# Performance work log

Measured on AMD Instinct MI355X. Metric: run time of the kernel, lower is better.

## Reference

```python
import jax, jax.numpy as jnp
import numpy as np


def setup_inputs() -> dict:
    key = jax.random.key(0)
    ks = jax.random.split(key, 5)
    B, S, D = 2, 2048, 1024
    std = 0.02
    return {
        "x": jax.random.normal(ks[0], (B, S, D), dtype=jnp.float32),
        "Wq": jax.random.normal(ks[1], (D, D), dtype=jnp.float32) * std,
        "Wk": jax.random.normal(ks[2], (D, D), dtype=jnp.float32) * std,
        "Wv": jax.random.normal(ks[3], (D, D), dtype=jnp.float32) * std,
        "Wo": jax.random.normal(ks[4], (D, D), dtype=jnp.float32) * std,
        "num_heads": 16,
        "window_size": 512,
    }


def reference(x, Wq, Wk, Wv, Wo, num_heads, window_size):
    B, S, D = x.shape
    H = num_heads
    d = D // H
    scale = d ** (-0.5)

    # QKV projections (torch Linear: y = x @ W.T), split heads -> b h s d
    def proj(W):
        return (x @ W.T).reshape(B, S, H, d).transpose(0, 2, 1, 3)

    q, k, v = proj(Wq), proj(Wk), proj(Wv)

    # [B, H, S, S] scores (faithful to the dense SDPA fallback)
    scores = jnp.einsum("bhsd,bhtd->bhst", q, k) * scale

    # sliding-window causal mask: col <= row and row - col < window_size
    pos = jnp.arange(S)
    row, col = pos[:, None], pos[None, :]
    mask = (col <= row) & (row - col < window_size)  # [S, S]
    scores = jnp.where(mask[None, None], scores, -jnp.inf)

    attn = jax.nn.softmax(scores, axis=-1)
    out = jnp.einsum("bhst,bhtd->bhsd", attn, v)  # b h s d
    out = out.transpose(0, 2, 1, 3).reshape(B, S, D)  # merge heads
    return out @ Wo.T
```

## Files before the change

### kernel.cpp

```cpp
#include <hip/hip_runtime.h>
#include <cstdint>

typedef uint16_t u16;
typedef __attribute__((ext_vector_type(8))) short short8;
typedef __attribute__((ext_vector_type(4))) float f32x4;

__device__ __forceinline__ u16 f2bf(float f) {
  uint32_t u = __float_as_uint(f);
  u += 0x7fff + ((u >> 16) & 1);
  return (u16)(u >> 16);
}
__device__ __forceinline__ uint32_t pk2bf(float a, float b) {
  uint32_t ua = __float_as_uint(a) + 0x8000u;
  uint32_t ub = __float_as_uint(b) + 0x8000u;
  return (ua >> 16) | (ub & 0xFFFF0000u);
}

#define GLL16(gp, lp) __builtin_amdgcn_global_load_lds( \
    (__attribute__((address_space(1))) void*)(gp), \
    (__attribute__((address_space(3))) void*)(lp), 16, 0, 0)

#define SBAR()       __builtin_amdgcn_s_barrier()
#define WAIT_LGKM0() asm volatile("s_waitcnt lgkmcnt(0)" ::: "memory")
#define WAIT_VM(N)   asm volatile("s_waitcnt vmcnt(" #N ")" ::: "memory")
#define MEMBAR()     asm volatile("" ::: "memory")

__global__ void cvt_all(const float* __restrict__ x,  const float* __restrict__ wq,
                        const float* __restrict__ wk, const float* __restrict__ wv,
                        const float* __restrict__ wo,
                        u16* __restrict__ xb, u16* __restrict__ wcat, u16* __restrict__ wob) {
  int i = blockIdx.x * 256 + threadIdx.x;
  const float4* src; ushort4* dst; int off; float sc = 1.0f;
  if (i < 1048576)      { src = (const float4*)x;  dst = (ushort4*)xb;              off = i; }
  else if (i < 1310720) { src = (const float4*)wq; dst = (ushort4*)wcat;            off = i - 1048576;
                          sc = 0.18033688011112042f; }
  else if (i < 1572864) { src = (const float4*)wk; dst = (ushort4*)wcat + 262144;   off = i - 1310720; }
  else if (i < 1835008) { src = (const float4*)wv; dst = (ushort4*)wcat + 524288;   off = i - 1572864; }
  else                  { src = (const float4*)wo; dst = (ushort4*)wob;             off = i - 1835008; }
  float4 v = src[off];
  ushort4 o;
  o.x = f2bf(v.x * sc); o.y = f2bf(v.y * sc); o.z = f2bf(v.z * sc); o.w = f2bf(v.w * sc);
  dst[off] = o;
}

template<int OUT_BF16>
__global__ __launch_bounds__(256, 2) void gemm128(const u16* __restrict__ A,
                                                  const u16* __restrict__ B,
                                                  void* __restrict__ Cout,
                                                  int N, int K, int ntN) {
  __shared__ u16 sm[2][2][128 * 64];
  const int tid  = threadIdx.x;
  const int lane = tid & 63, w = tid >> 6;
  const int wr = w >> 1, wc = w & 1;
  const int g = lane >> 4, lr = lane & 15;

  const int cpx = gridDim.x >> 3;
  const int id  = blockIdx.x;
  const int sw  = (id & 7) * cpx + (id >> 3);
  const int row0 = (sw / ntN) * 128, col0 = (sw % ntN) * 128;
  const int T = K >> 6;

  f32x4 acc[4][4];
  #pragma unroll
  for (int i = 0; i < 4; ++i)
    #pragma unroll
    for (int j = 0; j < 4; ++j) acc[i][j] = (f32x4){0.f, 0.f, 0.f, 0.f};

  auto STAGE = [&](int kt, int bufi) {
    #pragma unroll
    for (int ab = 0; ab < 2; ++ab) {
      const u16* __restrict__ src = ab ? B : A;
      const int rb = ab ? col0 : row0;
      #pragma unroll
      for (int j = 0; j < 4; ++j) {
        int r  = j * 32 + w * 8 + (lane >> 3);
        int sb = ((lane & 7) << 4) ^ ((r & 7) << 4);
        const u16* gp = src + (size_t)(rb + r) * K + kt * 64 + (sb >> 1);
        GLL16(gp, &sm[bufi][ab][(size_t)(j * 32 + w * 8) * 64]);
      }
    }
  };

  STAGE(0, 0); STAGE(1, 1);
  WAIT_VM(8); SBAR(); MEMBAR();

  for (int t = 0; t < T; ++t) {
    const int cur = t & 1;
    short8 a[4][2], b[4][2];
    #pragma unroll
    for (int mm = 0; mm < 4; ++mm)
      #pragma unroll
      for (int kh = 0; kh < 2; ++kh) {
        int row = wr * 64 + mm * 16 + lr;
        int col = (kh * 64 + g * 16) ^ ((row & 7) << 4);
        a[mm][kh] = *(const short8*)((const char*)&sm[cur][0][0] + row * 128 + col);
      }
    #pragma unroll
    for (int nn = 0; nn < 4; ++nn)
      #pragma unroll
      for (int kh = 0; kh < 2; ++kh) {
        int row = wc * 64 + nn * 16 + lr;
        int col = (kh * 64 + g * 16) ^ ((row & 7) << 4);
        b[nn][kh] = *(const short8*)((const char*)&sm[cur][1][0] + row * 128 + col);
      }
    WAIT_LGKM0(); MEMBAR(); SBAR(); MEMBAR();

    if (t + 2 < T) STAGE(t + 2, cur);

    __builtin_amdgcn_s_setprio(1);
    #pragma unroll
    for (int kh = 0; kh < 2; ++kh)
      #pragma unroll
      for (int mm = 0; mm < 4; ++mm)
        #pragma unroll
        for (int nn = 0; nn < 4; ++nn)
          acc[mm][nn] = __builtin_amdgcn_mfma_f32_16x16x32_bf16(
              a[mm][kh], b[nn][kh], acc[mm][nn], 0, 0, 0);
    __builtin_amdgcn_s_setprio(0);

    if (t + 1 < T) {
      if (t + 2 < T) { WAIT_VM(8); } else { WAIT_VM(0); }
      SBAR(); MEMBAR();
    }
  }

  #pragma unroll
  for (int i = 0; i < 4; ++i)
    #pragma unroll
    for (int j = 0; j < 4; ++j)
      #pragma unroll
      for (int ri = 0; ri < 4; ++ri) {
        int rr = row0 + wr * 64 + i * 16 + g * 4 + ri;
        int cc = col0 + wc * 64 + j * 16 + lr;
        if (OUT_BF16) ((u16*)Cout)[(size_t)rr * N + cc] = f2bf(acc[i][j][ri]);
        else          ((float*)Cout)[(size_t)rr * N + cc] = acc[i][j][ri];
      }
}

__global__ __launch_bounds__(256) void attn_swa(const u16* __restrict__ QKV, u16* __restrict__ O) {
  const int S = 2048;
  const int qb = blockIdx.x * 128;
  const int b = blockIdx.y >> 4, h = blockIdx.y & 15;
  const int tid = threadIdx.x;
  const int lane = tid & 63, w = tid >> 6;
  const int g = lane >> 4, lr = lane & 15;

  __shared__ u16 Klds[2][64 * 64];
  __shared__ u16 Vt[64][72];
  __shared__ u16 Plds[4][32][72];

  const u16* Qb = QKV + (size_t)b * S * 3072 + h * 64;
  const u16* Kb = QKV + (size_t)b * S * 3072 + 1024 + h * 64;
  const u16* Vb = QKV + (size_t)b * S * 3072 + 2048 + h * 64;

  const int qw = qb + w * 32;
  short8 qf[2][2];
  #pragma unroll
  for (int qg = 0; qg < 2; ++qg)
    #pragma unroll
    for (int kh = 0; kh < 2; ++kh)
      qf[qg][kh] = *(const short8*)(Qb + (size_t)(qw + qg * 16 + lr) * 3072 + kh * 32 + g * 8);

  float ls[2] = {0.f, 0.f};
  f32x4 accO[2][4];
  #pragma unroll
  for (int qg = 0; qg < 2; ++qg)
    #pragma unroll
    for (int i = 0; i < 4; ++i) accO[qg][i] = (f32x4){0.f, 0.f, 0.f, 0.f};

  int ks = qb - 511; if (ks < 0) ks = 0; ks &= ~63;
  const int ke = qb + 127;
  const int nt = ((ke - ks) >> 6) + 1;

  short8 vreg0, vreg1;

  auto STAGE_K = [&](int kb, int buf) {
    #pragma unroll
    for (int c = 0; c < 2; ++c) {
      int r  = c * 32 + w * 8 + (lane >> 3);
      int sb = ((lane & 7) << 4) ^ ((r & 7) << 4);
      const u16* gp = Kb + (size_t)(kb + r) * 3072 + (sb >> 1);
      u16* lp = Klds[buf] + c * 2048 + w * 512;
      GLL16(gp, lp);
    }
  };
  auto LOAD_V = [&](int kb) {
    vreg0 = *(const short8*)(Vb + (size_t)(kb + lane) * 3072 + w * 8);
    vreg1 = *(const short8*)(Vb + (size_t)(kb + lane) * 3072 + w * 8 + 32);
  };
  auto WRITE_V = [&]() {
    #pragma unroll
    for (int j = 0; j < 8; ++j) Vt[w * 8 + j][lane]      = (u16)vreg0[j];
    #pragma unroll
    for (int j = 0; j < 8; ++j) Vt[w * 8 + 32 + j][lane] = (u16)vreg1[j];
  };

  STAGE_K(ks, 0);
  LOAD_V(ks);
  __syncthreads();
  WRITE_V();
  __syncthreads();

  int cur = 0, kb = ks;
  for (int t = 0; t < nt; ++t, kb += 64) {
    const int nxt = cur ^ 1;
    const bool more = (t + 1 < nt);
    if (more) { STAGE_K(kb + 64, nxt); LOAD_V(kb + 64); }

    float p[2][4][4];
    #pragma unroll
    for (int st = 0; st < 4; ++st) {
      f32x4 c4[2];
      c4[0] = (f32x4){0.f, 0.f, 0.f, 0.f};
      c4[1] = (f32x4){0.f, 0.f, 0.f, 0.f};
      int r = st * 16 + lr;
      int swz = (r & 7) << 4;
      const char* krow = (const char*)(Klds[cur]) + r * 128;
      short8 kf0 = *(const short8*)(krow + ((g * 16) ^ swz));
      short8 kf1 = *(const short8*)(krow + ((64 + g * 16) ^ swz));
      __builtin_amdgcn_s_setprio(1);
      c4[0] = __builtin_amdgcn_mfma_f32_16x16x32_bf16(kf0, qf[0][0], c4[0], 0, 0, 0);
      c4[1] = __builtin_amdgcn_mfma_f32_16x16x32_bf16(kf0, qf[1][0], c4[1], 0, 0, 0);
      c4[0] = __builtin_amdgcn_mfma_f32_16x16x32_bf16(kf1, qf[0][1], c4[0], 0, 0, 0);
      c4[1] = __builtin_amdgcn_mfma_f32_16x16x32_bf16(kf1, qf[1][1], c4[1], 0, 0, 0);
      __builtin_amdgcn_s_setprio(0);
      #pragma unroll
      for (int ri = 0; ri < 4; ++ri) { p[0][st][ri] = c4[0][ri]; p[1][st][ri] = c4[1][ri]; }
    }

    #pragma unroll
    for (int qg = 0; qg < 2; ++qg) {
      const int q0 = qw + qg * 16;
      const bool clean = (kb + 63 <= q0) && (q0 + 15 - kb < 512);
      if (clean) {
        #pragma unroll
        for (int st = 0; st < 4; ++st)
          #pragma unroll
          for (int ri = 0; ri < 4; ++ri)
            p[qg][st][ri] = __builtin_amdgcn_exp2f(p[qg][st][ri]);
      } else {
        const int base = q0 + lr - kb;
        #pragma unroll
        for (int st = 0; st < 4; ++st)
          #pragma unroll
          for (int ri = 0; ri < 4; ++ri) {
            float e = __builtin_amdgcn_exp2f(p[qg][st][ri]);
            p[qg][st][ri] = ((uint32_t)(base - (st * 16 + g * 4 + ri)) < 512u) ? e : 0.f;
          }
      }
      float s = 0.f;
      #pragma unroll
      for (int st = 0; st < 4; ++st)
        #pragma unroll
        for (int ri = 0; ri < 4; ++ri) s += p[qg][st][ri];
      s += __shfl_xor(s, 16);
      s += __shfl_xor(s, 32);
      ls[qg] += s;

      #pragma unroll
      for (int st = 0; st < 4; ++st) {
        uint2 u2;
        u2.x = pk2bf(p[qg][st][0], p[qg][st][1]);
        u2.y = pk2bf(p[qg][st][2], p[qg][st][3]);
        *(uint2*)(&Plds[w][qg * 16 + lr][st * 16 + g * 4]) = u2;
      }
    }

    short8 pf[2][2];
    #pragma unroll
    for (int qg = 0; qg < 2; ++qg) {
      pf[qg][0] = *(const short8*)(&Plds[w][qg * 16 + lr][g * 8]);
      pf[qg][1] = *(const short8*)(&Plds[w][qg * 16 + lr][32 + g * 8]);
    }
    __builtin_amdgcn_s_setprio(1);
    #pragma unroll
    for (int dt = 0; dt < 4; ++dt) {
      short8 vf0 = *(const short8*)(&Vt[dt * 16 + lr][g * 8]);
      short8 vf1 = *(const short8*)(&Vt[dt * 16 + lr][32 + g * 8]);
      accO[0][dt] = __builtin_amdgcn_mfma_f32_16x16x32_bf16(pf[0][0], vf0, accO[0][dt], 0, 0, 0);
      accO[1][dt] = __builtin_amdgcn_mfma_f32_16x16x32_bf16(pf[1][0], vf0, accO[1][dt], 0, 0, 0);
      accO[0][dt] = __builtin_amdgcn_mfma_f32_16x16x32_bf16(pf[0][1], vf1, accO[0][dt], 0, 0, 0);
      accO[1][dt] = __builtin_amdgcn_mfma_f32_16x16x32_bf16(pf[1][1], vf1, accO[1][dt], 0, 0, 0);
    }
    __builtin_amdgcn_s_setprio(0);

    __syncthreads();
    if (more) WRITE_V();
    __syncthreads();
    cur = nxt;
  }

  #pragma unroll
  for (int qg = 0; qg < 2; ++qg) {
    float lsq[4];
    #pragma unroll
    for (int ri = 0; ri < 4; ++ri) lsq[ri] = __shfl(ls[qg], g * 4 + ri);
    #pragma unroll
    for (int dt = 0; dt < 4; ++dt)
      #pragma unroll
      for (int ri = 0; ri < 4; ++ri) {
        int qi = qw + qg * 16 + g * 4 + ri;
        O[(size_t)(b * S + qi) * 1024 + h * 64 + dt * 16 + lr] = f2bf(accO[qg][dt][ri] / lsq[ri]);
      }
  }
}

extern "C" void kernel_launch(void* const* d_in, const int* in_sizes, int n_in,
                              void* d_out, int out_size, void* d_ws, size_t ws_size,
                              hipStream_t stream) {
  const float* x  = (const float*)d_in[0];
  const float* Wq = (const float*)d_in[1];
  const float* Wk = (const float*)d_in[2];
  const float* Wv = (const float*)d_in[3];
  const float* Wo = (const float*)d_in[4];

  char* ws = (char*)d_ws;
  u16* xb   = (u16*)(ws);
  u16* Wcat = (u16*)(ws + (8  << 20));
  u16* Wob  = (u16*)(ws + (14 << 20));
  u16* QKV  = (u16*)(ws + (16 << 20));
  u16* Oatt = (u16*)(ws + (40 << 20));

  cvt_all<<<8192, 256, 0, stream>>>(x, Wq, Wk, Wv, Wo, xb, Wcat, Wob);
  gemm128<1><<<768, 256, 0, stream>>>(xb, Wcat, QKV, 3072, 1024, 24);
  attn_swa<<<dim3(16, 32), 256, 0, stream>>>(QKV, Oatt);
  gemm128<0><<<256, 256, 0, stream>>>(Oatt, Wob, d_out, 1024, 1024, 8);
}
```

Measured before the change: 91.01 us.

## Double-buffer V tile in LDS and drop one barrier per attention iteration

The transposed V tile in LDS is now double-buffered, so the next tile can be written while the current one is still being read. This removes the barrier that guarded the write-after-read and leaves a single barrier per iteration. The V global loads are reordered ahead of the K async LDS copies so that explicit vmcnt waits can target the V data alone. An occupancy hint of 3 blocks per CU is added to launch bounds. The extra LDS for the second V buffer and the register cap from the hint could limit occupancy or cause spills.

```diff
diff --git a/kernel.cpp b/kernel.cpp
--- a/kernel.cpp
+++ b/kernel.cpp
@@ -137,7 +137,7 @@
       }
 }
 
-__global__ __launch_bounds__(256) void attn_swa(const u16* __restrict__ QKV, u16* __restrict__ O) {
+__global__ __launch_bounds__(256, 3) void attn_swa(const u16* __restrict__ QKV, u16* __restrict__ O) {
   const int S = 2048;
   const int qb = blockIdx.x * 128;
   const int b = blockIdx.y >> 4, h = blockIdx.y & 15;
@@ -146,7 +146,7 @@
   const int g = lane >> 4, lr = lane & 15;
 
   __shared__ u16 Klds[2][64 * 64];
-  __shared__ u16 Vt[64][72];
+  __shared__ u16 Vt[2][64][72];
   __shared__ u16 Plds[4][32][72];
 
   const u16* Qb = QKV + (size_t)b * S * 3072 + h * 64;
@@ -188,24 +188,25 @@
     vreg0 = *(const short8*)(Vb + (size_t)(kb + lane) * 3072 + w * 8);
     vreg1 = *(const short8*)(Vb + (size_t)(kb + lane) * 3072 + w * 8 + 32);
   };
-  auto WRITE_V = [&]() {
-    #pragma unroll
-    for (int j = 0; j < 8; ++j) Vt[w * 8 + j][lane]      = (u16)vreg0[j];
-    #pragma unroll
-    for (int j = 0; j < 8; ++j) Vt[w * 8 + 32 + j][lane] = (u16)vreg1[j];
+  auto WRITE_V = [&](int buf) {
+    #pragma unroll
+    for (int j = 0; j < 8; ++j) Vt[buf][w * 8 + j][lane]      = (u16)vreg0[j];
+    #pragma unroll
+    for (int j = 0; j < 8; ++j) Vt[buf][w * 8 + 32 + j][lane] = (u16)vreg1[j];
   };
 
-  STAGE_K(ks, 0);
-  LOAD_V(ks);
-  __syncthreads();
-  WRITE_V();
-  __syncthreads();
+  LOAD_V(ks); MEMBAR();
+  STAGE_K(ks, 0); MEMBAR();
+  WAIT_VM(2); MEMBAR();
+  WRITE_V(0);
+  WAIT_VM(0); WAIT_LGKM0(); MEMBAR();
+  SBAR(); MEMBAR();
 
   int cur = 0, kb = ks;
   for (int t = 0; t < nt; ++t, kb += 64) {
     const int nxt = cur ^ 1;
     const bool more = (t + 1 < nt);
-    if (more) { STAGE_K(kb + 64, nxt); LOAD_V(kb + 64); }
+    if (more) { LOAD_V(kb + 64); MEMBAR(); STAGE_K(kb + 64, nxt); MEMBAR(); }
 
     float p[2][4][4];
     #pragma unroll
@@ -275,8 +276,8 @@
     __builtin_amdgcn_s_setprio(1);
     #pragma unroll
     for (int dt = 0; dt < 4; ++dt) {
-      short8 vf0 = *(const short8*)(&Vt[dt * 16 + lr][g * 8]);
-      short8 vf1 = *(const short8*)(&Vt[dt * 16 + lr][32 + g * 8]);
+      short8 vf0 = *(const short8*)(&Vt[cur][dt * 16 + lr][g * 8]);
+      short8 vf1 = *(const short8*)(&Vt[cur][dt * 16 + lr][32 + g * 8]);
       accO[0][dt] = __builtin_amdgcn_mfma_f32_16x16x32_bf16(pf[0][0], vf0, accO[0][dt], 0, 0, 0);
       accO[1][dt] = __builtin_amdgcn_mfma_f32_16x16x32_bf16(pf[1][0], vf0, accO[1][dt], 0, 0, 0);
       accO[0][dt] = __builtin_amdgcn_mfma_f32_16x16x32_bf16(pf[0][1], vf1, accO[0][dt], 0, 0, 0);
@@ -284,9 +285,12 @@
     }
     __builtin_amdgcn_s_setprio(0);
 
-    __syncthreads();
-    if (more) WRITE_V();
-    __syncthreads();
+    if (more) {
+      WAIT_VM(2); MEMBAR();
+      WRITE_V(nxt);
+      WAIT_VM(0); WAIT_LGKM0(); MEMBAR();
+      SBAR(); MEMBAR();
+    }
     cur = nxt;
   }
 
```

New measurement: 91.37 us. Within noise of the previous version (+0.4%).
